# Kernel optimization log

Hardware: AMD Instinct MI355X
Metric: run time of the kernel (lower is better)

The kernel has to match this reference:

```python
import jax, jax.numpy as jnp
import numpy as np
from jax import lax

B, N, R, L = 16, 256, 24, 32
MEAN_STOP_TIME_S = 60.0
AVG_TRANSFER_WAIT_TIME_S = 300.0
SYMMETRIC_ROUTES = True
INF = jnp.inf


def setup_inputs() -> dict:
    key = jax.random.key(0)
    k1, k2, k3 = jax.random.split(key, 3)
    drive_times = jax.random.uniform(k1, (B, N, N), jnp.float32) * 1000.0 + 30.0
    demand = jax.random.uniform(k2, (B, N, N), jnp.float32) * 10.0
    demand = demand * (1.0 - jnp.eye(N, dtype=jnp.float32))  # no self-demand
    batch_routes = jax.random.randint(k3, (B, R, L), 0, N, dtype=jnp.int32)
    return {"drive_times": drive_times, "demand": demand, "batch_routes": batch_routes}


def _route_edges_and_legs(routes, dtm):
    # routes: [B,R,L] node ids (no -1 padding in this setup); dtm: [B,N,N]
    b = jnp.arange(B)[:, None, None]
    sf, st = routes[:, :, :-1], routes[:, :, 1:]
    leg_fwd = dtm[b, sf, st] + MEAN_STOP_TIME_S            # [B,R,L-1]
    zero = jnp.zeros((B, R, 1), dtm.dtype)
    cum_f = jnp.concatenate([zero, jnp.cumsum(leg_fwd, -1)], -1)  # [B,R,L]
    tri = jnp.triu(jnp.ones((L, L), dtype=bool), 1)
    # ride time from stop position i to position j>i along the route
    t_f = jnp.where(tri, cum_f[:, :, None, :] - cum_f[:, :, :, None], INF)
    b4 = jnp.arange(B)[:, None, None, None]
    src = jnp.broadcast_to(routes[:, :, :, None], (B, R, L, L))
    dst = jnp.broadcast_to(routes[:, :, None, :], (B, R, L, L))
    edge = jnp.full((B, N, N), INF, dtm.dtype)
    edge = edge.at[b4, src, dst].min(t_f)
    leg_rev = None
    if SYMMETRIC_ROUTES:
        leg_rev = dtm[b, st, sf] + MEAN_STOP_TIME_S        # reverse-direction legs
        cum_r = jnp.concatenate([zero, jnp.cumsum(leg_rev, -1)], -1)
        t_r = jnp.where(tri, cum_r[:, :, None, :] - cum_r[:, :, :, None], INF)
        edge = edge.at[b4, dst, src].min(t_r)              # ride from s_j back to s_i
    return edge, leg_fwd, leg_rev


def _floyd_warshall(edge):
    # batched FW, also tracking hop count of shortest paths
    idx = jnp.arange(N)
    dist = edge.at[:, idx, idx].set(0.0)
    offdiag = ~jnp.eye(N, dtype=bool)
    hops = jnp.where(jnp.isfinite(dist) & offdiag, 1.0, 0.0)

    def body(carry, k):
        d, h = carry
        dc = lax.dynamic_slice_in_dim(d, k, 1, axis=2)  # [B,N,1]
        dr = lax.dynamic_slice_in_dim(d, k, 1, axis=1)  # [B,1,N]
        hc = lax.dynamic_slice_in_dim(h, k, 1, axis=2)
        hr = lax.dynamic_slice_in_dim(h, k, 1, axis=1)
        alt = dc + dr
        better = alt < d
        return (jnp.where(better, alt, d), jnp.where(better, hc + hr, h)), None

    (dist, hops), _ = lax.scan(body, (dist, hops), idx)
    return dist, hops


def reference(drive_times, demand, batch_routes):
    edge, leg_fwd, leg_rev = _route_edges_and_legs(batch_routes, drive_times)
    dist, hops = _floyd_warshall(edge)
    nopath = jnp.isinf(dist)
    path_lens = jnp.where(nopath, 0.0, hops + 1.0)  # n nodes on path (diag -> 1)
    transfers = jnp.where(path_lens == 0.0, 0.0, path_lens - 2.0)
    trip_times = jnp.where(nopath, 0.0, dist + transfers * AVG_TRANSFER_WAIT_TIME_S)
    total_demand_time = (demand * trip_times).sum((1, 2))
    total_transfers = (demand * transfers).sum((1, 2))
    unserved_demand = jnp.where(nopath, demand, 0.0).sum((1, 2))
    total_demand = demand.sum((1, 2))
    n_disconnected = (nopath & (demand > 0)).sum((1, 2))
    buckets = [jnp.where(transfers == float(ii), demand, 0.0).sum((1, 2)) for ii in range(3)]
    d_un = jnp.where(transfers > 2.0, demand, 0.0).sum((1, 2)) + unserved_demand
    trips_at_transfers = jnp.stack(buckets + [d_un], axis=1)  # [B,4]
    total_route_time = leg_fwd.sum((1, 2))
    if SYMMETRIC_ROUTES:
        total_route_time = total_route_time + leg_rev.sum((1, 2))
    return (total_demand_time, total_route_time, trips_at_transfers,
            total_demand, unserved_demand, total_transfers, trip_times,
            n_disconnected)
```

## Files before the change

### kernel.cpp

```cpp
#include <hip/hip_runtime.h>

#define BB 16
#define NL 256
#define RR 24
#define LL 32
#define NN (NL*NL)
#define BNN (BB*NN)
#define TT 64
#define NBLK 4

#define O_TDT 0
#define O_RT  16
#define O_TAT 32
#define O_TD  96
#define O_UNS 112
#define O_TTR 128
#define O_TT  144
#define O_ND  1048720

#define IDX4(r, ch) (((r)<<6) + ((((ch) ^ ((r)&15)))<<2))
#define LD4(A, r, ch) (*(float4*)&A[IDX4((r),(ch))])

static __device__ __forceinline__ void atomicMinF(float* a, float v){
    atomicMin((unsigned int*)a, __float_as_uint(v));
}

static __device__ __forceinline__ void fix4(float dv[4], float hv[4], int gi, int gj0){
    #pragma unroll
    for (int e = 0; e < 4; e++){
        int gj = gj0 + e;
        hv[e] = (gi != gj && dv[e] < 1e37f) ? 1.f : 0.f;
        if (gi == gj) dv[e] = 0.f;
    }
}

__global__ __launch_bounds__(1024) void k_init(float4* __restrict__ dist4, float* __restrict__ acc){
    int idx = blockIdx.x*1024 + threadIdx.x;
    float inf = __builtin_huge_valf();
    dist4[idx] = make_float4(inf, inf, inf, inf);
    if (blockIdx.x == 0 && threadIdx.x < 256) acc[threadIdx.x] = 0.f;
}

__global__ void k_routes(const float* __restrict__ dtm, const int* __restrict__ routes,
                         float* __restrict__ dist, float* __restrict__ acc){
    int br = blockIdx.x; int b = br / RR, r = br % RR;
    int lane = threadIdx.x;
    __shared__ int   s[LL];
    __shared__ float lf[LL], lr[LL], cf[LL], cr[LL];
    if (lane < LL) s[lane] = routes[(b*RR + r)*LL + lane];
    __syncthreads();
    if (lane < LL-1){
        int a0 = s[lane], a1 = s[lane+1];
        const float* dt = dtm + b*NN;
        lf[lane] = dt[a0*NL + a1] + 60.0f;
        lr[lane] = dt[a1*NL + a0] + 60.0f;
    }
    __syncthreads();
    if (lane == 0){
        float af = 0.f, ar = 0.f;
        cf[0] = 0.f; cr[0] = 0.f;
        for (int l = 0; l < LL-1; l++){
            af += lf[l]; ar += lr[l];
            cf[l+1] = af; cr[l+1] = ar;
        }
        atomicAdd(&acc[b*16 + 1], af + ar);
    }
    __syncthreads();
    for (int p = lane; p < LL*LL; p += 64){
        int i = p >> 5, j = p & 31;
        if (j > i){
            atomicMinF(&dist[b*NN + s[i]*NL + s[j]], cf[j] - cf[i]);
            atomicMinF(&dist[b*NN + s[j]*NL + s[i]], cr[j] - cr[i]);
        }
    }
}

__global__ __launch_bounds__(512) void k_fw_round(
        const float* __restrict__ srcD, const float* __restrict__ srcH,
        float* __restrict__ dstD, float* __restrict__ dstH, int kb, int dofix){
    int b  = blockIdx.y;
    int m  = blockIdx.x;
    int ti = m >> 2, tj = m & 3;
    int t  = threadIdx.x;
    int rp  = (t >> 4) * 2;
    int cch = t & 15;
    int c04 = cch * 4;
    __shared__ float KD[4096], KH[4096];
    __shared__ float BD[4096], BH[4096];
    const float* Kg  = srcD + b*NN + kb*TT*(NL+1);
    const float* KgH = srcH + b*NN + kb*TT*(NL+1);
    const float* Bg  = srcD + b*NN + kb*TT*NL + tj*TT;
    const float* BgH = srcH + b*NN + kb*TT*NL + tj*TT;
    const float* Cg  = srcD + b*NN + ti*TT*NL + kb*TT;
    const float* CgH = srcH + b*NN + ti*TT*NL + kb*TT;
    const float* Dg  = srcD + b*NN + ti*TT*NL + tj*TT;
    const float* DgH = srcH + b*NN + ti*TT*NL + tj*TT;

    #pragma unroll
    for (int u = 0; u < 2; u++){
        int fid = u*512 + t;
        int row = fid >> 4, ch = fid & 15, c4 = ch*4;
        float4 v = *(const float4*)(Kg + row*NL + c4);
        float kd[4] = {v.x,v.y,v.z,v.w}, kh[4];
        float4 w = *(const float4*)(Bg + row*NL + c4);
        float bd[4] = {w.x,w.y,w.z,w.w}, bh[4];
        if (dofix){
            fix4(kd, kh, kb*TT+row, kb*TT+c4);
            fix4(bd, bh, kb*TT+row, tj*TT+c4);
        } else {
            float4 q = *(const float4*)(KgH + row*NL + c4);
            kh[0]=q.x; kh[1]=q.y; kh[2]=q.z; kh[3]=q.w;
            float4 r2 = *(const float4*)(BgH + row*NL + c4);
            bh[0]=r2.x; bh[1]=r2.y; bh[2]=r2.z; bh[3]=r2.w;
        }
        LD4(KD,row,ch) = make_float4(kd[0],kd[1],kd[2],kd[3]);
        LD4(KH,row,ch) = make_float4(kh[0],kh[1],kh[2],kh[3]);
        LD4(BD,row,ch) = make_float4(bd[0],bd[1],bd[2],bd[3]);
        LD4(BH,row,ch) = make_float4(bh[0],bh[1],bh[2],bh[3]);
    }
    __syncthreads();

    for (int skb = 0; skb < 4; skb++){
        int s0 = skb*16, sch = skb*4;
        if (t < 64){
            int i = t >> 2, jg = t & 3;
            int base = IDX4(s0+i, sch+jg);
            float md[4], mh[4];
            #pragma unroll
            for (int c = 0; c < 4; c++){ md[c] = KD[base+c]; mh[c] = KH[base+c]; }
            #pragma unroll
            for (int k = 0; k < 16; k++){
                float rd[4], rh[4];
                #pragma unroll
                for (int c = 0; c < 4; c++){
                    rd[c] = __shfl(md[c], (k<<2)|jg);
                    rh[c] = __shfl(mh[c], (k<<2)|jg);
                }
                float cd = __shfl(md[k&3], (i<<2)|(k>>2));
                float ch = __shfl(mh[k&3], (i<<2)|(k>>2));
                #pragma unroll
                for (int c = 0; c < 4; c++){
                    float alt = cd + rd[c];
                    if (alt < md[c]){ md[c] = alt; mh[c] = ch + rh[c]; }
                }
            }
            #pragma unroll
            for (int c = 0; c < 4; c++){ KD[base+c] = md[c]; KH[base+c] = mh[c]; }
        }
        __syncthreads();
        float sd[4], sh[4];
        int wrow, wch;
        if (t < 256){
            int rsr = s0 + (t >> 4);
            wrow = rsr; wch = t & 15;
            float4 v = LD4(KD, rsr, wch), w = LD4(KH, rsr, wch);
            sd[0]=v.x; sd[1]=v.y; sd[2]=v.z; sd[3]=v.w;
            sh[0]=w.x; sh[1]=w.y; sh[2]=w.z; sh[3]=w.w;
            #pragma unroll
            for (int k = 0; k < 16; k++){
                int kch = sch + (k>>2), ko = k & 3;
                float ad = KD[IDX4(rsr,kch)+ko], ah = KH[IDX4(rsr,kch)+ko];
                float4 bv = LD4(KD, s0+k, wch), bq = LD4(KH, s0+k, wch);
                float bd[4]={bv.x,bv.y,bv.z,bv.w}, bh[4]={bq.x,bq.y,bq.z,bq.w};
                #pragma unroll
                for (int e = 0; e < 4; e++){
                    float alt = ad + bd[e];
                    if (alt < sd[e]){ sd[e] = alt; sh[e] = ah + bh[e]; }
                }
            }
        } else {
            int t2 = t - 256;
            int csr = t2 >> 2;
            wrow = csr; wch = sch + (t2 & 3);
            float4 v = LD4(KD, csr, wch), w = LD4(KH, csr, wch);
            sd[0]=v.x; sd[1]=v.y; sd[2]=v.z; sd[3]=v.w;
            sh[0]=w.x; sh[1]=w.y; sh[2]=w.z; sh[3]=w.w;
            #pragma unroll
            for (int k = 0; k < 16; k++){
                int kch = sch + (k>>2), ko = k & 3;
                float a2 = KD[IDX4(csr,kch)+ko], a2h = KH[IDX4(csr,kch)+ko];
                float4 bv = LD4(KD, s0+k, wch), bq = LD4(KH, s0+k, wch);
                float bd[4]={bv.x,bv.y,bv.z,bv.w}, bh[4]={bq.x,bq.y,bq.z,bq.w};
                #pragma unroll
                for (int e = 0; e < 4; e++){
                    float alt = a2 + bd[e];
                    if (alt < sd[e]){ sd[e] = alt; sh[e] = a2h + bh[e]; }
                }
            }
        }
        __syncthreads();
        LD4(KD, wrow, wch) = make_float4(sd[0],sd[1],sd[2],sd[3]);
        LD4(KH, wrow, wch) = make_float4(sh[0],sh[1],sh[2],sh[3]);
        __syncthreads();
        float dd[2][4], hh[2][4];
        #pragma unroll
        for (int i = 0; i < 2; i++){
            float4 v = LD4(KD, rp+i, cch), w = LD4(KH, rp+i, cch);
            dd[i][0]=v.x; dd[i][1]=v.y; dd[i][2]=v.z; dd[i][3]=v.w;
            hh[i][0]=w.x; hh[i][1]=w.y; hh[i][2]=w.z; hh[i][3]=w.w;
        }
        #pragma unroll
        for (int q4 = 0; q4 < 4; q4++){
            int kch = sch + q4, kr = s0 + q4*4;
            float a[2][4], ah[2][4], bm[4][4], bh[4][4];
            #pragma unroll
            for (int i = 0; i < 2; i++){
                float4 av = LD4(KD, rp+i, kch), aq = LD4(KH, rp+i, kch);
                a[i][0]=av.x; a[i][1]=av.y; a[i][2]=av.z; a[i][3]=av.w;
                ah[i][0]=aq.x; ah[i][1]=aq.y; ah[i][2]=aq.z; ah[i][3]=aq.w;
            }
            #pragma unroll
            for (int q = 0; q < 4; q++){
                float4 bv = LD4(KD, kr+q, cch), bq = LD4(KH, kr+q, cch);
                bm[q][0]=bv.x; bm[q][1]=bv.y; bm[q][2]=bv.z; bm[q][3]=bv.w;
                bh[q][0]=bq.x; bh[q][1]=bq.y; bh[q][2]=bq.z; bh[q][3]=bq.w;
            }
            #pragma unroll
            for (int q = 0; q < 4; q++)
            #pragma unroll
            for (int i = 0; i < 2; i++)
            #pragma unroll
            for (int j = 0; j < 4; j++){
                float alt = a[i][q] + bm[q][j];
                if (alt < dd[i][j]){ dd[i][j] = alt; hh[i][j] = ah[i][q] + bh[q][j]; }
            }
        }
        __syncthreads();
        #pragma unroll
        for (int i = 0; i < 2; i++){
            LD4(KD, rp+i, cch) = make_float4(dd[i][0],dd[i][1],dd[i][2],dd[i][3]);
            LD4(KH, rp+i, cch) = make_float4(hh[i][0],hh[i][1],hh[i][2],hh[i][3]);
        }
        __syncthreads();
    }

    float inf = __builtin_huge_valf();
    float md[2][4], mh[2][4];
    #pragma unroll
    for (int i = 0; i < 2; i++)
    #pragma unroll
    for (int j = 0; j < 4; j++){ md[i][j] = inf; mh[i][j] = 0.f; }
    #pragma unroll 4
    for (int q4 = 0; q4 < 16; q4++){
        int kr = q4*4;
        float a[2][4], ah[2][4], bm[4][4], bh[4][4];
        #pragma unroll
        for (int i = 0; i < 2; i++){
            float4 av = LD4(KD, rp+i, q4), aq = LD4(KH, rp+i, q4);
            a[i][0]=av.x; a[i][1]=av.y; a[i][2]=av.z; a[i][3]=av.w;
            ah[i][0]=aq.x; ah[i][1]=aq.y; ah[i][2]=aq.z; ah[i][3]=aq.w;
        }
        #pragma unroll
        for (int q = 0; q < 4; q++){
            float4 bv = LD4(BD, kr+q, cch), bq = LD4(BH, kr+q, cch);
            bm[q][0]=bv.x; bm[q][1]=bv.y; bm[q][2]=bv.z; bm[q][3]=bv.w;
            bh[q][0]=bq.x; bh[q][1]=bq.y; bh[q][2]=bq.z; bh[q][3]=bq.w;
        }
        #pragma unroll
        for (int q = 0; q < 4; q++)
        #pragma unroll
        for (int i = 0; i < 2; i++)
        #pragma unroll
        for (int j = 0; j < 4; j++){
            float alt = a[i][q] + bm[q][j];
            if (alt < md[i][j]){ md[i][j] = alt; mh[i][j] = ah[i][q] + bh[q][j]; }
        }
    }
    __syncthreads();
    #pragma unroll
    for (int i = 0; i < 2; i++){
        LD4(BD, rp+i, cch) = make_float4(md[i][0],md[i][1],md[i][2],md[i][3]);
        LD4(BH, rp+i, cch) = make_float4(mh[i][0],mh[i][1],mh[i][2],mh[i][3]);
        float4 cv = *(const float4*)(Cg + (rp+i)*NL + c04);
        float cd[4] = {cv.x,cv.y,cv.z,cv.w}, chv[4];
        if (dofix){
            fix4(cd, chv, ti*TT+rp+i, kb*TT+c04);
        } else {
            float4 cq = *(const float4*)(CgH + (rp+i)*NL + c04);
            chv[0]=cq.x; chv[1]=cq.y; chv[2]=cq.z; chv[3]=cq.w;
        }
        LD4(KD, rp+i, cch) = make_float4(cd[0],cd[1],cd[2],cd[3]);
        LD4(KH, rp+i, cch) = make_float4(chv[0],chv[1],chv[2],chv[3]);
    }
    __syncthreads();

    float dd[2][4], hh[2][4];
    #pragma unroll
    for (int i = 0; i < 2; i++){
        float4 v = *(const float4*)(Dg + (rp+i)*NL + c04);
        float dv[4] = {v.x,v.y,v.z,v.w}, hv[4];
        if (dofix){
            fix4(dv, hv, ti*TT+rp+i, tj*TT+c04);
        } else {
            float4 w = *(const float4*)(DgH + (rp+i)*NL + c04);
            hv[0]=w.x; hv[1]=w.y; hv[2]=w.z; hv[3]=w.w;
        }
        #pragma unroll
        for (int e = 0; e < 4; e++){ dd[i][e] = dv[e]; hh[i][e] = hv[e]; }
    }
    #pragma unroll 4
    for (int q4 = 0; q4 < 16; q4++){
        int kr = q4*4;
        float a[2][4], ah[2][4], bm[4][4], bh[4][4];
        #pragma unroll
        for (int i = 0; i < 2; i++){
            float4 av = LD4(KD, rp+i, q4), aq = LD4(KH, rp+i, q4);
            a[i][0]=av.x; a[i][1]=av.y; a[i][2]=av.z; a[i][3]=av.w;
            ah[i][0]=aq.x; ah[i][1]=aq.y; ah[i][2]=aq.z; ah[i][3]=aq.w;
        }
        #pragma unroll
        for (int q = 0; q < 4; q++){
            float4 bv = LD4(BD, kr+q, cch), bq = LD4(BH, kr+q, cch);
            bm[q][0]=bv.x; bm[q][1]=bv.y; bm[q][2]=bv.z; bm[q][3]=bv.w;
            bh[q][0]=bq.x; bh[q][1]=bq.y; bh[q][2]=bq.z; bh[q][3]=bq.w;
        }
        #pragma unroll
        for (int q = 0; q < 4; q++)
        #pragma unroll
        for (int i = 0; i < 2; i++)
        #pragma unroll
        for (int j = 0; j < 4; j++){
            float alt = a[i][q] + bm[q][j];
            if (alt < dd[i][j]){ dd[i][j] = alt; hh[i][j] = ah[i][q] + bh[q][j]; }
        }
    }
    float* Od = dstD + b*NN + ti*TT*NL + tj*TT;
    float* Oh = dstH + b*NN + ti*TT*NL + tj*TT;
    #pragma unroll
    for (int i = 0; i < 2; i++){
        *(float4*)(Od + (rp+i)*NL + c04) = make_float4(dd[i][0],dd[i][1],dd[i][2],dd[i][3]);
        *(float4*)(Oh + (rp+i)*NL + c04) = make_float4(hh[i][0],hh[i][1],hh[i][2],hh[i][3]);
    }
}

__global__ __launch_bounds__(1024) void k_epi(const float4* __restrict__ dist4,
        const float4* __restrict__ hops4, const float4* __restrict__ demand4,
        float* __restrict__ out, float* __restrict__ acc){
    int b = blockIdx.y;
    int fid = (b*NN >> 2) + blockIdx.x*1024 + threadIdx.x;
    float4 dv = dist4[fid], hv = hops4[fid], mv = demand4[fid];
    float ds[4] = {dv.x,dv.y,dv.z,dv.w};
    float hs[4] = {hv.x,hv.y,hv.z,hv.w};
    float ms[4] = {mv.x,mv.y,mv.z,mv.w};
    float s0=0,s1=0,s2=0,s3=0,s4=0,s5=0,s6=0,s7=0,s8=0;
    float tts[4];
    #pragma unroll
    for (int e = 0; e < 4; e++){
        float d = ds[e], h = hs[e], dm = ms[e];
        bool np = !(d < 1e37f);
        float pl = np ? 0.f : h + 1.f;
        float tr = (pl == 0.f) ? 0.f : pl - 2.f;
        float tt = np ? 0.f : d + tr*300.f;
        tts[e] = tt;
        s0 += dm*tt;
        s1 += dm*tr;
        s2 += np ? dm : 0.f;
        s3 += dm;
        s4 += (np && dm > 0.f) ? 1.f : 0.f;
        s5 += (tr == 0.f) ? dm : 0.f;
        s6 += (tr == 1.f) ? dm : 0.f;
        s7 += (tr == 2.f) ? dm : 0.f;
        s8 += (tr > 2.f) ? dm : 0.f;
    }
    ((float4*)(out + O_TT))[fid] = make_float4(tts[0],tts[1],tts[2],tts[3]);
    #define RED(x) { x += __shfl_down(x,32); x += __shfl_down(x,16); x += __shfl_down(x,8); \
                     x += __shfl_down(x,4);  x += __shfl_down(x,2);  x += __shfl_down(x,1); }
    RED(s0) RED(s1) RED(s2) RED(s3) RED(s4) RED(s5) RED(s6) RED(s7) RED(s8)
    __shared__ float red[16][9];
    int w = threadIdx.x >> 6;
    if ((threadIdx.x & 63) == 0){
        red[w][0]=s0; red[w][1]=s1; red[w][2]=s2; red[w][3]=s3; red[w][4]=s4;
        red[w][5]=s5; red[w][6]=s6; red[w][7]=s7; red[w][8]=s8;
    }
    __syncthreads();
    if (threadIdx.x < 9){
        float v = 0.f;
        #pragma unroll
        for (int ww = 0; ww < 16; ww++) v += red[ww][threadIdx.x];
        int slot = (threadIdx.x == 0) ? 0 : threadIdx.x + 1;
        atomicAdd(&acc[b*16 + slot], v);
    }
    __syncthreads();
    __shared__ int isLast;
    if (threadIdx.x == 0){
        unsigned prev = atomicAdd((unsigned int*)(acc + 255), 1u);
        isLast = (prev == 255u) ? 1 : 0;
    }
    __syncthreads();
    if (isLast && threadIdx.x < BB){
        int bb = threadIdx.x;
        float a[10];
        #pragma unroll
        for (int s = 0; s < 10; s++) a[s] = atomicAdd(&acc[bb*16 + s], 0.f);
        out[O_TDT + bb] = a[0];
        out[O_RT  + bb] = a[1];
        out[O_TAT + 4*bb + 0] = a[6];
        out[O_TAT + 4*bb + 1] = a[7];
        out[O_TAT + 4*bb + 2] = a[8];
        out[O_TAT + 4*bb + 3] = a[9] + a[3];
        out[O_TD  + bb] = a[4];
        out[O_UNS + bb] = a[3];
        out[O_TTR + bb] = a[2];
        out[O_ND  + bb] = a[5];
    }
}

extern "C" void kernel_launch(void* const* d_in, const int* in_sizes, int n_in,
                              void* d_out, int out_size, void* d_ws, size_t ws_size,
                              hipStream_t stream){
    (void)in_sizes; (void)n_in; (void)out_size; (void)ws_size;
    const float* dtm    = (const float*)d_in[0];
    const float* demand = (const float*)d_in[1];
    const int*   routes = (const int*)d_in[2];
    float* out   = (float*)d_out;
    float* distA = (float*)d_ws;
    float* hopsA = distA + BNN;
    float* distB = hopsA + BNN;
    float* hopsB = distB + BNN;
    float* acc   = hopsB + BNN;

    k_init  <<<BNN/4096, 1024, 0, stream>>>((float4*)distA, acc);
    k_routes<<<BB*RR,      64, 0, stream>>>(dtm, routes, distA, acc);
    k_fw_round<<<dim3(16,BB), 512, 0, stream>>>(distA, hopsA, distB, hopsB, 0, 1);
    k_fw_round<<<dim3(16,BB), 512, 0, stream>>>(distB, hopsB, distA, hopsA, 1, 0);
    k_fw_round<<<dim3(16,BB), 512, 0, stream>>>(distA, hopsA, distB, hopsB, 2, 0);
    k_fw_round<<<dim3(16,BB), 512, 0, stream>>>(distB, hopsB, distA, hopsA, 3, 0);
    k_epi<<<dim3(16,BB), 1024, 0, stream>>>((const float4*)distA, (const float4*)hopsA,
                                            (const float4*)demand, out, acc);
}
```

Baseline: 286.4 us.

## Pack distance and hop count into one double, use fmin-based Floyd-Warshall

Replaces the separate float distance and hop-count matrices with a single double per entry. Each edge weight gets a tiny 2^-30 increment so the low-order mantissa bits accumulate the hop count as paths are summed. The inner relaxations become plain fmin on doubles instead of compare-and-select over two arrays, and the diagonal fix moves into the init kernel. This halves the matrix count, but every element is now 8 bytes and uses FP64 adds. It also risks precision or tie-breaking differences from the packed hop encoding.

```diff
diff --git a/kernel.cpp b/kernel.cpp
--- a/kernel.cpp
+++ b/kernel.cpp
@@ -7,7 +7,6 @@
 #define NN (NL*NL)
 #define BNN (BB*NN)
 #define TT 64
-#define NBLK 4
 
 #define O_TDT 0
 #define O_RT  16
@@ -18,31 +17,27 @@
 #define O_TT  144
 #define O_ND  1048720
 
-#define IDX4(r, ch) (((r)<<6) + ((((ch) ^ ((r)&15)))<<2))
-#define LD4(A, r, ch) (*(float4*)&A[IDX4((r),(ch))])
-
-static __device__ __forceinline__ void atomicMinF(float* a, float v){
-    atomicMin((unsigned int*)a, __float_as_uint(v));
-}
-
-static __device__ __forceinline__ void fix4(float dv[4], float hv[4], int gi, int gj0){
-    #pragma unroll
-    for (int e = 0; e < 4; e++){
-        int gj = gj0 + e;
-        hv[e] = (gi != gj && dv[e] < 1e37f) ? 1.f : 0.f;
-        if (gi == gj) dv[e] = 0.f;
-    }
-}
-
-__global__ __launch_bounds__(1024) void k_init(float4* __restrict__ dist4, float* __restrict__ acc){
+#define HSC 9.3132257461547852e-10
+#define H2  1073741824.0
+#define HMASK 8191
+
+#define RIDX(r, c2) (((r)<<6) + ((((c2) ^ ((r)&31)))<<1))
+#define LDD(A, r, c2) (*(double2*)&A[RIDX((r),(c2))])
+
+__global__ __launch_bounds__(1024) void k_init(double2* __restrict__ dist2, float* __restrict__ acc){
     int idx = blockIdx.x*1024 + threadIdx.x;
-    float inf = __builtin_huge_valf();
-    dist4[idx] = make_float4(inf, inf, inf, inf);
+    double inf = __builtin_huge_val();
+    double2 v = make_double2(inf, inf);
+    int q = (idx*2) & (NN-1);
+    int r = q % 257;
+    if (r == 0)   v.x = 0.0;
+    if (r == 256) v.y = 0.0;
+    dist2[idx] = v;
     if (blockIdx.x == 0 && threadIdx.x < 256) acc[threadIdx.x] = 0.f;
 }
 
 __global__ void k_routes(const float* __restrict__ dtm, const int* __restrict__ routes,
-                         float* __restrict__ dist, float* __restrict__ acc){
+                         unsigned long long* __restrict__ dist, float* __restrict__ acc){
     int br = blockIdx.x; int b = br / RR, r = br % RR;
     int lane = threadIdx.x;
     __shared__ int   s[LL];
@@ -69,15 +64,16 @@
     for (int p = lane; p < LL*LL; p += 64){
         int i = p >> 5, j = p & 31;
         if (j > i){
-            atomicMinF(&dist[b*NN + s[i]*NL + s[j]], cf[j] - cf[i]);
-            atomicMinF(&dist[b*NN + s[j]*NL + s[i]], cr[j] - cr[i]);
+            double vf = (double)(cf[j] - cf[i]) + HSC;
+            double vr = (double)(cr[j] - cr[i]) + HSC;
+            atomicMin(&dist[b*NN + s[i]*NL + s[j]], (unsigned long long)__double_as_longlong(vf));
+            atomicMin(&dist[b*NN + s[j]*NL + s[i]], (unsigned long long)__double_as_longlong(vr));
         }
     }
 }
 
 __global__ __launch_bounds__(512) void k_fw_round(
-        const float* __restrict__ srcD, const float* __restrict__ srcH,
-        float* __restrict__ dstD, float* __restrict__ dstH, int kb, int dofix){
+        const double* __restrict__ src, double* __restrict__ dst, int kb){
     int b  = blockIdx.y;
     int m  = blockIdx.x;
     int ti = m >> 2, tj = m & 3;
@@ -85,270 +81,222 @@
     int rp  = (t >> 4) * 2;
     int cch = t & 15;
     int c04 = cch * 4;
-    __shared__ float KD[4096], KH[4096];
-    __shared__ float BD[4096], BH[4096];
-    const float* Kg  = srcD + b*NN + kb*TT*(NL+1);
-    const float* KgH = srcH + b*NN + kb*TT*(NL+1);
-    const float* Bg  = srcD + b*NN + kb*TT*NL + tj*TT;
-    const float* BgH = srcH + b*NN + kb*TT*NL + tj*TT;
-    const float* Cg  = srcD + b*NN + ti*TT*NL + kb*TT;
-    const float* CgH = srcH + b*NN + ti*TT*NL + kb*TT;
-    const float* Dg  = srcD + b*NN + ti*TT*NL + tj*TT;
-    const float* DgH = srcH + b*NN + ti*TT*NL + tj*TT;
+    __shared__ double KD[4096];
+    __shared__ double BD[4096];
+    const double* Kg = src + b*NN + kb*TT*(NL+1);
+    const double* Bg = src + b*NN + kb*TT*NL + tj*TT;
+    const double* Cg = src + b*NN + ti*TT*NL + kb*TT;
+    const double* Dg = src + b*NN + ti*TT*NL + tj*TT;
+
+    double c0[2][4], d0[2][4];
+    #pragma unroll
+    for (int i = 0; i < 2; i++){
+        double2 ca = *(const double2*)(Cg + (rp+i)*NL + c04);
+        double2 cb = *(const double2*)(Cg + (rp+i)*NL + c04 + 2);
+        c0[i][0]=ca.x; c0[i][1]=ca.y; c0[i][2]=cb.x; c0[i][3]=cb.y;
+        double2 da = *(const double2*)(Dg + (rp+i)*NL + c04);
+        double2 db = *(const double2*)(Dg + (rp+i)*NL + c04 + 2);
+        d0[i][0]=da.x; d0[i][1]=da.y; d0[i][2]=db.x; d0[i][3]=db.y;
+    }
 
     #pragma unroll
     for (int u = 0; u < 2; u++){
         int fid = u*512 + t;
-        int row = fid >> 4, ch = fid & 15, c4 = ch*4;
-        float4 v = *(const float4*)(Kg + row*NL + c4);
-        float kd[4] = {v.x,v.y,v.z,v.w}, kh[4];
-        float4 w = *(const float4*)(Bg + row*NL + c4);
-        float bd[4] = {w.x,w.y,w.z,w.w}, bh[4];
-        if (dofix){
-            fix4(kd, kh, kb*TT+row, kb*TT+c4);
-            fix4(bd, bh, kb*TT+row, tj*TT+c4);
-        } else {
-            float4 q = *(const float4*)(KgH + row*NL + c4);
-            kh[0]=q.x; kh[1]=q.y; kh[2]=q.z; kh[3]=q.w;
-            float4 r2 = *(const float4*)(BgH + row*NL + c4);
-            bh[0]=r2.x; bh[1]=r2.y; bh[2]=r2.z; bh[3]=r2.w;
-        }
-        LD4(KD,row,ch) = make_float4(kd[0],kd[1],kd[2],kd[3]);
-        LD4(KH,row,ch) = make_float4(kh[0],kh[1],kh[2],kh[3]);
-        LD4(BD,row,ch) = make_float4(bd[0],bd[1],bd[2],bd[3]);
-        LD4(BH,row,ch) = make_float4(bh[0],bh[1],bh[2],bh[3]);
+        int row = fid >> 4, cc = fid & 15;
+        const double* kp = Kg + row*NL + cc*4;
+        double2 k0 = *(const double2*)kp, k1 = *(const double2*)(kp+2);
+        const double* bp = Bg + row*NL + cc*4;
+        double2 b0 = *(const double2*)bp, b1 = *(const double2*)(bp+2);
+        LDD(KD,row,cc*2)   = k0; LDD(KD,row,cc*2+1) = k1;
+        LDD(BD,row,cc*2)   = b0; LDD(BD,row,cc*2+1) = b1;
     }
     __syncthreads();
 
     for (int skb = 0; skb < 4; skb++){
-        int s0 = skb*16, sch = skb*4;
+        int s0 = skb*16, sc2 = skb*8;
         if (t < 64){
-            int i = t >> 2, jg = t & 3;
-            int base = IDX4(s0+i, sch+jg);
-            float md[4], mh[4];
-            #pragma unroll
-            for (int c = 0; c < 4; c++){ md[c] = KD[base+c]; mh[c] = KH[base+c]; }
+            int i = t >> 2, jg = t & 3, rr = s0 + i, cb = sc2 + jg*2;
+            double2 m0 = LDD(KD, rr, cb), m1 = LDD(KD, rr, cb+1);
+            double md[4] = {m0.x, m0.y, m1.x, m1.y};
             #pragma unroll
             for (int k = 0; k < 16; k++){
-                float rd[4], rh[4];
+                double rd[4];
                 #pragma unroll
-                for (int c = 0; c < 4; c++){
-                    rd[c] = __shfl(md[c], (k<<2)|jg);
-                    rh[c] = __shfl(mh[c], (k<<2)|jg);
-                }
-                float cd = __shfl(md[k&3], (i<<2)|(k>>2));
-                float ch = __shfl(mh[k&3], (i<<2)|(k>>2));
+                for (int c = 0; c < 4; c++) rd[c] = __shfl(md[c], (k<<2)|jg);
+                double cd = __shfl(md[k&3], (i<<2)|(k>>2));
                 #pragma unroll
-                for (int c = 0; c < 4; c++){
-                    float alt = cd + rd[c];
-                    if (alt < md[c]){ md[c] = alt; mh[c] = ch + rh[c]; }
-                }
-            }
-            #pragma unroll
-            for (int c = 0; c < 4; c++){ KD[base+c] = md[c]; KH[base+c] = mh[c]; }
-        }
-        __syncthreads();
-        float sd[4], sh[4];
-        int wrow, wch;
+                for (int c = 0; c < 4; c++) md[c] = fmin(md[c], cd + rd[c]);
+            }
+            LDD(KD, rr, cb)   = make_double2(md[0], md[1]);
+            LDD(KD, rr, cb+1) = make_double2(md[2], md[3]);
+        }
+        __syncthreads();
+        double sd[4];
+        int wrow, wc2;
         if (t < 256){
             int rsr = s0 + (t >> 4);
-            wrow = rsr; wch = t & 15;
-            float4 v = LD4(KD, rsr, wch), w = LD4(KH, rsr, wch);
-            sd[0]=v.x; sd[1]=v.y; sd[2]=v.z; sd[3]=v.w;
-            sh[0]=w.x; sh[1]=w.y; sh[2]=w.z; sh[3]=w.w;
+            wrow = rsr; wc2 = (t & 15)*2;
+            double2 v0 = LDD(KD, rsr, wc2), v1 = LDD(KD, rsr, wc2+1);
+            sd[0]=v0.x; sd[1]=v0.y; sd[2]=v1.x; sd[3]=v1.y;
             #pragma unroll
             for (int k = 0; k < 16; k++){
-                int kch = sch + (k>>2), ko = k & 3;
-                float ad = KD[IDX4(rsr,kch)+ko], ah = KH[IDX4(rsr,kch)+ko];
-                float4 bv = LD4(KD, s0+k, wch), bq = LD4(KH, s0+k, wch);
-                float bd[4]={bv.x,bv.y,bv.z,bv.w}, bh[4]={bq.x,bq.y,bq.z,bq.w};
-                #pragma unroll
-                for (int e = 0; e < 4; e++){
-                    float alt = ad + bd[e];
-                    if (alt < sd[e]){ sd[e] = alt; sh[e] = ah + bh[e]; }
-                }
+                double ad = KD[RIDX(rsr, sc2+(k>>1)) + (k&1)];
+                double2 b0 = LDD(KD, s0+k, wc2), b1 = LDD(KD, s0+k, wc2+1);
+                sd[0] = fmin(sd[0], ad + b0.x);
+                sd[1] = fmin(sd[1], ad + b0.y);
+                sd[2] = fmin(sd[2], ad + b1.x);
+                sd[3] = fmin(sd[3], ad + b1.y);
             }
         } else {
             int t2 = t - 256;
             int csr = t2 >> 2;
-            wrow = csr; wch = sch + (t2 & 3);
-            float4 v = LD4(KD, csr, wch), w = LD4(KH, csr, wch);
-            sd[0]=v.x; sd[1]=v.y; sd[2]=v.z; sd[3]=v.w;
-            sh[0]=w.x; sh[1]=w.y; sh[2]=w.z; sh[3]=w.w;
+            wrow = csr; wc2 = sc2 + (t2 & 3)*2;
+            double2 v0 = LDD(KD, csr, wc2), v1 = LDD(KD, csr, wc2+1);
+            sd[0]=v0.x; sd[1]=v0.y; sd[2]=v1.x; sd[3]=v1.y;
             #pragma unroll
             for (int k = 0; k < 16; k++){
-                int kch = sch + (k>>2), ko = k & 3;
-                float a2 = KD[IDX4(csr,kch)+ko], a2h = KH[IDX4(csr,kch)+ko];
-                float4 bv = LD4(KD, s0+k, wch), bq = LD4(KH, s0+k, wch);
-                float bd[4]={bv.x,bv.y,bv.z,bv.w}, bh[4]={bq.x,bq.y,bq.z,bq.w};
-                #pragma unroll
-                for (int e = 0; e < 4; e++){
-                    float alt = a2 + bd[e];
-                    if (alt < sd[e]){ sd[e] = alt; sh[e] = a2h + bh[e]; }
-                }
-            }
-        }
-        __syncthreads();
-        LD4(KD, wrow, wch) = make_float4(sd[0],sd[1],sd[2],sd[3]);
-        LD4(KH, wrow, wch) = make_float4(sh[0],sh[1],sh[2],sh[3]);
-        __syncthreads();
-        float dd[2][4], hh[2][4];
+                double ad = KD[RIDX(csr, sc2+(k>>1)) + (k&1)];
+                double2 b0 = LDD(KD, s0+k, wc2), b1 = LDD(KD, s0+k, wc2+1);
+                sd[0] = fmin(sd[0], ad + b0.x);
+                sd[1] = fmin(sd[1], ad + b0.y);
+                sd[2] = fmin(sd[2], ad + b1.x);
+                sd[3] = fmin(sd[3], ad + b1.y);
+            }
+        }
+        __syncthreads();
+        LDD(KD, wrow, wc2)   = make_double2(sd[0], sd[1]);
+        LDD(KD, wrow, wc2+1) = make_double2(sd[2], sd[3]);
+        __syncthreads();
+        double dd[2][4];
         #pragma unroll
         for (int i = 0; i < 2; i++){
-            float4 v = LD4(KD, rp+i, cch), w = LD4(KH, rp+i, cch);
-            dd[i][0]=v.x; dd[i][1]=v.y; dd[i][2]=v.z; dd[i][3]=v.w;
-            hh[i][0]=w.x; hh[i][1]=w.y; hh[i][2]=w.z; hh[i][3]=w.w;
+            double2 v0 = LDD(KD, rp+i, cch*2), v1 = LDD(KD, rp+i, cch*2+1);
+            dd[i][0]=v0.x; dd[i][1]=v0.y; dd[i][2]=v1.x; dd[i][3]=v1.y;
         }
         #pragma unroll
         for (int q4 = 0; q4 < 4; q4++){
-            int kch = sch + q4, kr = s0 + q4*4;
-            float a[2][4], ah[2][4], bm[4][4], bh[4][4];
+            double a[2][4], bm[4][4];
             #pragma unroll
             for (int i = 0; i < 2; i++){
-                float4 av = LD4(KD, rp+i, kch), aq = LD4(KH, rp+i, kch);
-                a[i][0]=av.x; a[i][1]=av.y; a[i][2]=av.z; a[i][3]=av.w;
-                ah[i][0]=aq.x; ah[i][1]=aq.y; ah[i][2]=aq.z; ah[i][3]=aq.w;
-            }
+                double2 a0 = LDD(KD, rp+i, sc2+q4*2), a1 = LDD(KD, rp+i, sc2+q4*2+1);
+                a[i][0]=a0.x; a[i][1]=a0.y; a[i][2]=a1.x; a[i][3]=a1.y;
+            }
+            int kr = s0 + q4*4;
             #pragma unroll
             for (int q = 0; q < 4; q++){
-                float4 bv = LD4(KD, kr+q, cch), bq = LD4(KH, kr+q, cch);
-                bm[q][0]=bv.x; bm[q][1]=bv.y; bm[q][2]=bv.z; bm[q][3]=bv.w;
-                bh[q][0]=bq.x; bh[q][1]=bq.y; bh[q][2]=bq.z; bh[q][3]=bq.w;
+                double2 b0 = LDD(KD, kr+q, cch*2), b1 = LDD(KD, kr+q, cch*2+1);
+                bm[q][0]=b0.x; bm[q][1]=b0.y; bm[q][2]=b1.x; bm[q][3]=b1.y;
             }
             #pragma unroll
             for (int q = 0; q < 4; q++)
             #pragma unroll
             for (int i = 0; i < 2; i++)
             #pragma unroll
-            for (int j = 0; j < 4; j++){
-                float alt = a[i][q] + bm[q][j];
-                if (alt < dd[i][j]){ dd[i][j] = alt; hh[i][j] = ah[i][q] + bh[q][j]; }
-            }
+            for (int j = 0; j < 4; j++)
+                dd[i][j] = fmin(dd[i][j], a[i][q] + bm[q][j]);
         }
         __syncthreads();
         #pragma unroll
         for (int i = 0; i < 2; i++){
-            LD4(KD, rp+i, cch) = make_float4(dd[i][0],dd[i][1],dd[i][2],dd[i][3]);
-            LD4(KH, rp+i, cch) = make_float4(hh[i][0],hh[i][1],hh[i][2],hh[i][3]);
-        }
-        __syncthreads();
-    }
-
-    float inf = __builtin_huge_valf();
-    float md[2][4], mh[2][4];
+            LDD(KD, rp+i, cch*2)   = make_double2(dd[i][0], dd[i][1]);
+            LDD(KD, rp+i, cch*2+1) = make_double2(dd[i][2], dd[i][3]);
+        }
+        __syncthreads();
+    }
+
+    double inf = __builtin_huge_val();
+    double md[2][4];
     #pragma unroll
     for (int i = 0; i < 2; i++)
     #pragma unroll
-    for (int j = 0; j < 4; j++){ md[i][j] = inf; mh[i][j] = 0.f; }
+    for (int j = 0; j < 4; j++) md[i][j] = inf;
     #pragma unroll 4
     for (int q4 = 0; q4 < 16; q4++){
+        double a[2][4], bm[4][4];
+        #pragma unroll
+        for (int i = 0; i < 2; i++){
+            double2 a0 = LDD(KD, rp+i, q4*2), a1 = LDD(KD, rp+i, q4*2+1);
+            a[i][0]=a0.x; a[i][1]=a0.y; a[i][2]=a1.x; a[i][3]=a1.y;
+        }
         int kr = q4*4;
-        float a[2][4], ah[2][4], bm[4][4], bh[4][4];
-        #pragma unroll
-        for (int i = 0; i < 2; i++){
-            float4 av = LD4(KD, rp+i, q4), aq = LD4(KH, rp+i, q4);
-            a[i][0]=av.x; a[i][1]=av.y; a[i][2]=av.z; a[i][3]=av.w;
-            ah[i][0]=aq.x; ah[i][1]=aq.y; ah[i][2]=aq.z; ah[i][3]=aq.w;
-        }
         #pragma unroll
         for (int q = 0; q < 4; q++){
-            float4 bv = LD4(BD, kr+q, cch), bq = LD4(BH, kr+q, cch);
-            bm[q][0]=bv.x; bm[q][1]=bv.y; bm[q][2]=bv.z; bm[q][3]=bv.w;
-            bh[q][0]=bq.x; bh[q][1]=bq.y; bh[q][2]=bq.z; bh[q][3]=bq.w;
+            double2 b0 = LDD(BD, kr+q, cch*2), b1 = LDD(BD, kr+q, cch*2+1);
+            bm[q][0]=b0.x; bm[q][1]=b0.y; bm[q][2]=b1.x; bm[q][3]=b1.y;
         }
         #pragma unroll
         for (int q = 0; q < 4; q++)
         #pragma unroll
         for (int i = 0; i < 2; i++)
         #pragma unroll
-        for (int j = 0; j < 4; j++){
-            float alt = a[i][q] + bm[q][j];
-            if (alt < md[i][j]){ md[i][j] = alt; mh[i][j] = ah[i][q] + bh[q][j]; }
-        }
+        for (int j = 0; j < 4; j++)
+            md[i][j] = fmin(md[i][j], a[i][q] + bm[q][j]);
     }
     __syncthreads();
     #pragma unroll
     for (int i = 0; i < 2; i++){
-        LD4(BD, rp+i, cch) = make_float4(md[i][0],md[i][1],md[i][2],md[i][3]);
-        LD4(BH, rp+i, cch) = make_float4(mh[i][0],mh[i][1],mh[i][2],mh[i][3]);
-        float4 cv = *(const float4*)(Cg + (rp+i)*NL + c04);
-        float cd[4] = {cv.x,cv.y,cv.z,cv.w}, chv[4];
-        if (dofix){
-            fix4(cd, chv, ti*TT+rp+i, kb*TT+c04);
-        } else {
-            float4 cq = *(const float4*)(CgH + (rp+i)*NL + c04);
-            chv[0]=cq.x; chv[1]=cq.y; chv[2]=cq.z; chv[3]=cq.w;
-        }
-        LD4(KD, rp+i, cch) = make_float4(cd[0],cd[1],cd[2],cd[3]);
-        LD4(KH, rp+i, cch) = make_float4(chv[0],chv[1],chv[2],chv[3]);
-    }
-    __syncthreads();
-
-    float dd[2][4], hh[2][4];
-    #pragma unroll
-    for (int i = 0; i < 2; i++){
-        float4 v = *(const float4*)(Dg + (rp+i)*NL + c04);
-        float dv[4] = {v.x,v.y,v.z,v.w}, hv[4];
-        if (dofix){
-            fix4(dv, hv, ti*TT+rp+i, tj*TT+c04);
-        } else {
-            float4 w = *(const float4*)(DgH + (rp+i)*NL + c04);
-            hv[0]=w.x; hv[1]=w.y; hv[2]=w.z; hv[3]=w.w;
-        }
-        #pragma unroll
-        for (int e = 0; e < 4; e++){ dd[i][e] = dv[e]; hh[i][e] = hv[e]; }
-    }
+        LDD(BD, rp+i, cch*2)   = make_double2(md[i][0], md[i][1]);
+        LDD(BD, rp+i, cch*2+1) = make_double2(md[i][2], md[i][3]);
+        LDD(KD, rp+i, cch*2)   = make_double2(c0[i][0], c0[i][1]);
+        LDD(KD, rp+i, cch*2+1) = make_double2(c0[i][2], c0[i][3]);
+    }
+    __syncthreads();
+
+    double dd[2][4];
+    #pragma unroll
+    for (int i = 0; i < 2; i++)
+    #pragma unroll
+    for (int j = 0; j < 4; j++) dd[i][j] = d0[i][j];
     #pragma unroll 4
     for (int q4 = 0; q4 < 16; q4++){
+        double a[2][4], bm[4][4];
+        #pragma unroll
+        for (int i = 0; i < 2; i++){
+            double2 a0 = LDD(KD, rp+i, q4*2), a1 = LDD(KD, rp+i, q4*2+1);
+            a[i][0]=a0.x; a[i][1]=a0.y; a[i][2]=a1.x; a[i][3]=a1.y;
+        }
         int kr = q4*4;
-        float a[2][4], ah[2][4], bm[4][4], bh[4][4];
-        #pragma unroll
-        for (int i = 0; i < 2; i++){
-            float4 av = LD4(KD, rp+i, q4), aq = LD4(KH, rp+i, q4);
-            a[i][0]=av.x; a[i][1]=av.y; a[i][2]=av.z; a[i][3]=av.w;
-            ah[i][0]=aq.x; ah[i][1]=aq.y; ah[i][2]=aq.z; ah[i][3]=aq.w;
-        }
         #pragma unroll
         for (int q = 0; q < 4; q++){
-            float4 bv = LD4(BD, kr+q, cch), bq = LD4(BH, kr+q, cch);
-            bm[q][0]=bv.x; bm[q][1]=bv.y; bm[q][2]=bv.z; bm[q][3]=bv.w;
-            bh[q][0]=bq.x; bh[q][1]=bq.y; bh[q][2]=bq.z; bh[q][3]=bq.w;
+            double2 b0 = LDD(BD, kr+q, cch*2), b1 = LDD(BD, kr+q, cch*2+1);
+            bm[q][0]=b0.x; bm[q][1]=b0.y; bm[q][2]=b1.x; bm[q][3]=b1.y;
         }
         #pragma unroll
         for (int q = 0; q < 4; q++)
         #pragma unroll
         for (int i = 0; i < 2; i++)
         #pragma unroll
-        for (int j = 0; j < 4; j++){
-            float alt = a[i][q] + bm[q][j];
-            if (alt < dd[i][j]){ dd[i][j] = alt; hh[i][j] = ah[i][q] + bh[q][j]; }
-        }
-    }
-    float* Od = dstD + b*NN + ti*TT*NL + tj*TT;
-    float* Oh = dstH + b*NN + ti*TT*NL + tj*TT;
+        for (int j = 0; j < 4; j++)
+            dd[i][j] = fmin(dd[i][j], a[i][q] + bm[q][j]);
+    }
+    double* Od = dst + b*NN + ti*TT*NL + tj*TT;
     #pragma unroll
     for (int i = 0; i < 2; i++){
-        *(float4*)(Od + (rp+i)*NL + c04) = make_float4(dd[i][0],dd[i][1],dd[i][2],dd[i][3]);
-        *(float4*)(Oh + (rp+i)*NL + c04) = make_float4(hh[i][0],hh[i][1],hh[i][2],hh[i][3]);
-    }
-}
-
-__global__ __launch_bounds__(1024) void k_epi(const float4* __restrict__ dist4,
-        const float4* __restrict__ hops4, const float4* __restrict__ demand4,
-        float* __restrict__ out, float* __restrict__ acc){
+        *(double2*)(Od + (rp+i)*NL + c04)     = make_double2(dd[i][0], dd[i][1]);
+        *(double2*)(Od + (rp+i)*NL + c04 + 2) = make_double2(dd[i][2], dd[i][3]);
+    }
+}
+
+__global__ __launch_bounds__(1024) void k_epi(const double2* __restrict__ dist2,
+        const float4* __restrict__ demand4, float* __restrict__ out, float* __restrict__ acc){
     int b = blockIdx.y;
     int fid = (b*NN >> 2) + blockIdx.x*1024 + threadIdx.x;
-    float4 dv = dist4[fid], hv = hops4[fid], mv = demand4[fid];
-    float ds[4] = {dv.x,dv.y,dv.z,dv.w};
-    float hs[4] = {hv.x,hv.y,hv.z,hv.w};
-    float ms[4] = {mv.x,mv.y,mv.z,mv.w};
+    long long q2 = (long long)fid * 2;
+    double2 va = dist2[q2], vb = dist2[q2+1];
+    double vs[4] = {va.x, va.y, vb.x, vb.y};
+    float4 mv = demand4[fid];
+    float ms[4] = {mv.x, mv.y, mv.z, mv.w};
     float s0=0,s1=0,s2=0,s3=0,s4=0,s5=0,s6=0,s7=0,s8=0;
     float tts[4];
     #pragma unroll
     for (int e = 0; e < 4; e++){
-        float d = ds[e], h = hs[e], dm = ms[e];
-        bool np = !(d < 1e37f);
-        float pl = np ? 0.f : h + 1.f;
+        double v = vs[e];
+        bool np = !(v < 1e37);
+        double vv = np ? 0.0 : v;
+        int h = (int)(((long long)(vv * H2)) & (long long)HMASK);
+        float d = (float)vv;
+        float dm = ms[e];
+        float pl = np ? 0.f : (float)(h + 1);
         float tr = (pl == 0.f) ? 0.f : pl - 2.f;
         float tt = np ? 0.f : d + tr*300.f;
         tts[e] = tt;
@@ -413,18 +361,16 @@
     const float* demand = (const float*)d_in[1];
     const int*   routes = (const int*)d_in[2];
     float* out   = (float*)d_out;
-    float* distA = (float*)d_ws;
-    float* hopsA = distA + BNN;
-    float* distB = hopsA + BNN;
-    float* hopsB = distB + BNN;
-    float* acc   = hopsB + BNN;
-
-    k_init  <<<BNN/4096, 1024, 0, stream>>>((float4*)distA, acc);
-    k_routes<<<BB*RR,      64, 0, stream>>>(dtm, routes, distA, acc);
-    k_fw_round<<<dim3(16,BB), 512, 0, stream>>>(distA, hopsA, distB, hopsB, 0, 1);
-    k_fw_round<<<dim3(16,BB), 512, 0, stream>>>(distB, hopsB, distA, hopsA, 1, 0);
-    k_fw_round<<<dim3(16,BB), 512, 0, stream>>>(distA, hopsA, distB, hopsB, 2, 0);
-    k_fw_round<<<dim3(16,BB), 512, 0, stream>>>(distB, hopsB, distA, hopsA, 3, 0);
-    k_epi<<<dim3(16,BB), 1024, 0, stream>>>((const float4*)distA, (const float4*)hopsA,
+    double* distA = (double*)d_ws;
+    double* distB = distA + BNN;
+    float*  acc   = (float*)(distB + BNN);
+
+    k_init  <<<512, 1024, 0, stream>>>((double2*)distA, acc);
+    k_routes<<<BB*RR,  64, 0, stream>>>(dtm, routes, (unsigned long long*)distA, acc);
+    k_fw_round<<<dim3(16,BB), 512, 0, stream>>>(distA, distB, 0);
+    k_fw_round<<<dim3(16,BB), 512, 0, stream>>>(distB, distA, 1);
+    k_fw_round<<<dim3(16,BB), 512, 0, stream>>>(distA, distB, 2);
+    k_fw_round<<<dim3(16,BB), 512, 0, stream>>>(distB, distA, 3);
+    k_epi<<<dim3(16,BB), 1024, 0, stream>>>((const double2*)distA,
                                             (const float4*)demand, out, acc);
 }
```

Measured after the change: 238.4 us. 16.7% less time.
